# Kernel tuning notes

Hardware: AMD Instinct MI355X
Metric: run time of the kernel (lower is better)

Reference implementation:

```python
import jax, jax.numpy as jnp
import numpy as np

WSZ = 8          # window size (h == w)
DIM_HEAD = 32
EPS = 1e-5


def _rotate_half(t):
    t1, t2 = jnp.split(t, 2, axis=-1)
    return jnp.concatenate([-t2, t1], axis=-1)


def _window_rope(wsz_h, wsz_w, dim_head, base=10000.0):
    quarter = dim_head // 4
    freq = 1.0 / base ** (jnp.arange(quarter, dtype=jnp.float32) / quarter)
    th = jnp.arange(wsz_h, dtype=jnp.float32)[:, None] * freq[None, :]   # (wh, q)
    tw = jnp.arange(wsz_w, dtype=jnp.float32)[:, None] * freq[None, :]   # (ww, q)
    th = jnp.broadcast_to(th[:, None, :], (wsz_h, wsz_w, quarter)).reshape(wsz_h * wsz_w, quarter)
    tw = jnp.broadcast_to(tw[None, :, :], (wsz_h, wsz_w, quarter)).reshape(wsz_h * wsz_w, quarter)
    theta = jnp.concatenate([th, tw], axis=-1)                            # (L, d/2)
    cos = jnp.concatenate([jnp.cos(theta), jnp.cos(theta)], axis=-1)      # (L, d)
    sin = jnp.concatenate([jnp.sin(theta), jnp.sin(theta)], axis=-1)
    return cos, sin


def setup_inputs() -> dict:
    key = jax.random.key(0)
    k1, k2, k3 = jax.random.split(key, 3)
    B, D, H, W = 4, 512, 128, 128
    inner = 512  # heads * dim_head
    return {
        "x": jax.random.normal(k1, (B, D, H, W), dtype=jnp.float32),
        "ln_g": jnp.ones((D,), jnp.float32),
        "ln_b": jnp.zeros((D,), jnp.float32),
        "w_qkv": jax.random.normal(k2, (3 * inner, D), jnp.float32) * 0.02,
        "w_out": jax.random.normal(k3, (D, inner), jnp.float32) * 0.02,
        "b_out": jnp.zeros((D,), jnp.float32),
    }


def reference(x, ln_g, ln_b, w_qkv, w_out, b_out):
    B, D, H, W = x.shape
    wsz = WSZ
    dh = DIM_HEAD
    heads = D // dh
    nh, nw = H // wsz, W // wsz
    L = wsz * wsz
    shift = wsz // 2

    # channel LayerNorm (biased var over dim=1)
    mean = jnp.mean(x, axis=1, keepdims=True)
    var = jnp.var(x, axis=1, keepdims=True)
    xn = (x - mean) / jnp.sqrt(var + EPS) * ln_g[None, :, None, None] + ln_b[None, :, None, None]

    # shifted windows
    xs = jnp.roll(xn, shift=(-shift, -shift), axis=(-2, -1))
    # b d (h s1) (w s2) -> (b h w) d s1 s2
    xw = xs.reshape(B, D, nh, wsz, nw, wsz).transpose(0, 2, 4, 1, 3, 5)
    xw = xw.reshape(B * nh * nw, D, wsz, wsz)

    # 1x1 conv qkv (no bias)
    qkv = jnp.einsum('bdxy,ed->bexy', xw, w_qkv)           # (Bw, 3*inner, ws, ws)
    q, k, v = jnp.split(qkv, 3, axis=1)

    def to_heads(t):
        Bw = t.shape[0]
        return t.reshape(Bw, heads, dh, L).transpose(0, 1, 3, 2)  # (Bw, h, L, d)
    q, k, v = map(to_heads, (q, k, v))

    cos, sin = _window_rope(wsz, wsz, dh)
    cos = cos[None, None].astype(q.dtype)
    sin = sin[None, None].astype(q.dtype)
    q = q * cos + _rotate_half(q) * sin
    k = k * cos + _rotate_half(k) * sin

    scale = dh ** -0.5
    logits = jnp.einsum('bhid,bhjd->bhij', q, k) * scale
    attn = jax.nn.softmax(logits, axis=-1)
    out = jnp.einsum('bhij,bhjd->bhid', attn, v)            # (Bw, h, L, d)

    # b h (x y) d -> b (h d) x y
    out = out.transpose(0, 1, 3, 2).reshape(B * nh * nw, heads * dh, wsz, wsz)
    out = jnp.einsum('bdxy,ed->bexy', out, w_out) + b_out[None, :, None, None]

    # (b h w) d s1 s2 -> b d (h s1) (w s2)
    out = out.reshape(B, nh, nw, D, wsz, wsz).transpose(0, 3, 1, 4, 2, 5)
    out = out.reshape(B, D, H, W)
    out = jnp.roll(out, shift=(shift, shift), axis=(-2, -1))
    return out
```

## Files before the change

### kernel.cpp

```cpp
#include <hip/hip_runtime.h>
#include <hip/hip_bf16.h>

typedef unsigned short u16;
typedef __attribute__((ext_vector_type(8))) __bf16 bf16x8;
typedef __attribute__((ext_vector_type(4))) float f32x4;
typedef __attribute__((ext_vector_type(8))) unsigned short u16x8;

#define DEV __device__ __forceinline__

DEV float bf2f(u16 v){ union{unsigned u; float f;} c; c.u=((unsigned)v)<<16; return c.f; }
DEV u16 f2bf(float f){ union{float f; unsigned u;} c; c.f=f; unsigned r=c.u+0x7FFFu+((c.u>>16)&1u); return (u16)(r>>16); }
DEV f32x4 mfma16(bf16x8 a, bf16x8 b, f32x4 c){ return __builtin_amdgcn_mfma_f32_16x16x32_bf16(a,b,c,0,0,0); }


__global__ __launch_bounds__(256) void cvt_params_k(const float* __restrict__ wqkv, const float* __restrict__ wout,
                                                    const float* __restrict__ bout,
                                                    u16* __restrict__ wqkv_c, u16* __restrict__ wout_c,
                                                    u16* __restrict__ bout_c){
  int i = blockIdx.x*256 + threadIdx.x;
  if (i < 786432) wqkv_c[i] = f2bf(wqkv[i]);
  int j = i - 786432;
  if (j >= 0 && j < 262144) wout_c[j] = f2bf(wout[j]);
  int k = i - 1048576;
  if (k >= 0 && k < 512) bout_c[k] = f2bf(bout[k]);
}

__global__ __launch_bounds__(256) void ln_fused_k(const float* __restrict__ x, const float* __restrict__ g,
                                                  const float* __restrict__ bta, u16* __restrict__ A){
  __shared__ float sb[4][64], qb[4][64];
  const int blk = blockIdx.x;
  const int b = blk >> 8, rem = blk & 255;
  const int h_src = rem >> 1, w0 = (rem & 1) << 6;
  const int tid = threadIdx.x, dg = tid >> 6, lp = tid & 63;
  const float* xp = x + (((size_t)b*512)*128 + h_src)*128 + w0 + lp;
  const int dbase = dg*128;

  float s = 0.f, q = 0.f;
  #pragma unroll 8
  for (int d = 0; d < 128; ++d){
    float v = xp[(size_t)(dbase + d)*16384];
    s += v; q += v*v;
  }
  sb[dg][lp] = s; qb[dg][lp] = q;
  __syncthreads();
  float ts = sb[0][lp]+sb[1][lp]+sb[2][lp]+sb[3][lp];
  float tq = qb[0][lp]+qb[1][lp]+qb[2][lp]+qb[3][lp];
  float mean = ts*(1.f/512.f);
  float rstd = rsqrtf(tq*(1.f/512.f) - mean*mean + 1e-5f);

  const int w_src = w0 + lp;
  const int h_out = (h_src - 4) & 127, w_out = (w_src - 4) & 127;
  const int m = ((b*16 + (h_out>>3))*16 + (w_out>>3))*64 + (h_out&7)*8 + (w_out&7);
  u16* orow = A + (size_t)m*512 + dbase;

  for (int d0 = 0; d0 < 128; d0 += 8){
    u16x8 o;
    #pragma unroll
    for (int j = 0; j < 8; ++j){
      int d = dbase + d0 + j;
      float v = xp[(size_t)d*16384];
      o[j] = f2bf((v - mean)*rstd*g[d] + bta[d]);
    }
    *(u16x8*)(orow + d0) = o;
  }
}

template<bool BIAS>
__global__ __launch_bounds__(256) void gemm_nt_k(const u16* __restrict__ A, const u16* __restrict__ B,
                                                 const u16* __restrict__ bias, u16* __restrict__ C,
                                                 int M, int N, int K){
  __shared__ u16 As[128*32];
  __shared__ u16 Bs[128*32];
  const int tid = threadIdx.x, lane = tid & 63, wv = tid >> 6;
  const int q4 = lane >> 4, cc = lane & 15;
  const int m0 = blockIdx.y*128, n0 = blockIdx.x*128;
  const int wm = (wv >> 1)*64, wn = (wv & 1)*64;

  const int lrow = tid >> 2, lgrp = tid & 3;
  const u16* ag0 = A + (size_t)(m0 + lrow)*K + lgrp*8;
  const u16* ag1 = ag0 + (size_t)64*K;
  const u16* bg0 = B + (size_t)(n0 + lrow)*K + lgrp*8;
  const u16* bg1 = bg0 + (size_t)64*K;
  u16* as0 = As + tid*8;  u16* as1 = As + 2048 + tid*8;
  u16* bs0 = Bs + tid*8;  u16* bs1 = Bs + 2048 + tid*8;

  f32x4 acc[4][4] = {};
  for (int k0 = 0; k0 < K; k0 += 32){
    __builtin_amdgcn_global_load_lds(ag0 + k0, as0, 16, 0, 0);
    __builtin_amdgcn_global_load_lds(ag1 + k0, as1, 16, 0, 0);
    __builtin_amdgcn_global_load_lds(bg0 + k0, bs0, 16, 0, 0);
    __builtin_amdgcn_global_load_lds(bg1 + k0, bs1, 16, 0, 0);
    __syncthreads();
    bf16x8 af[4], bfr[4];
    #pragma unroll
    for (int t=0; t<4; ++t){
      u16x8 ta = *(const u16x8*)(As + (wm + t*16 + cc)*32 + q4*8);
      af[t]  = __builtin_bit_cast(bf16x8, ta);
      u16x8 tb = *(const u16x8*)(Bs + (wn + t*16 + cc)*32 + q4*8);
      bfr[t] = __builtin_bit_cast(bf16x8, tb);
    }
    #pragma unroll
    for (int i=0; i<4; ++i)
      #pragma unroll
      for (int j=0; j<4; ++j)
        acc[i][j] = mfma16(af[i], bfr[j], acc[i][j]);
    __syncthreads();
  }
  #pragma unroll
  for (int j=0; j<4; ++j){
    int col = n0 + wn + j*16 + cc;
    float bv = 0.f;
    if (BIAS) bv = bf2f(bias[col]);
    #pragma unroll
    for (int i=0; i<4; ++i){
      int rbase = m0 + wm + i*16 + q4*4;
      #pragma unroll
      for (int r=0; r<4; ++r)
        C[(size_t)(rbase + r)*N + col] = f2bf(acc[i][j][r] + bv);
    }
  }
}

__global__ __launch_bounds__(256) void attn_k(const u16* __restrict__ qkv, u16* __restrict__ O){
  __shared__ u16 Psh[4][64*72];
  const int tid = threadIdx.x, lane = tid & 63, wv = tid >> 6;
  const int q4 = lane >> 4, cc = lane & 15;
  const int w0 = blockIdx.x;
  const size_t base = (size_t)w0*64*1536;
  u16* Pw = Psh[wv];

  float freqj[8];
  #pragma unroll
  for (int j=0; j<8; ++j) freqj[j] = exp2f(-1.6609640474436811f * (float)j);
  const float sgn = (q4 < 2) ? -1.f : 1.f;
  const bool use_s2 = (q4 & 1) != 0;

  for (int hh=0; hh<4; ++hh){
    const int h = wv*4 + hh;
    bf16x8 qf[4], kf[4];
    #pragma unroll
    for (int t=0; t<4; ++t){
      const int l = t*16 + cc;
      const float sel = use_s2 ? (float)(l & 7) : (float)(l >> 3);
      u16x8 qr = *(const u16x8*)(qkv + base + (size_t)l*1536 + h*32 + q4*8);
      u16x8 kr = *(const u16x8*)(qkv + base + (size_t)l*1536 + 512 + h*32 + q4*8);
      u16x8 qo, ko;
      #pragma unroll
      for (int j=0; j<8; ++j){
        float qv = bf2f(qr[j]), kv = bf2f(kr[j]);
        float qp = __shfl_xor(qv, 32);
        float kp = __shfl_xor(kv, 32);
        float sn, cs; __sincosf(sel * freqj[j], &sn, &cs);
        qo[j] = f2bf(qv*cs + sgn*qp*sn);
        ko[j] = f2bf(kv*cs + sgn*kp*sn);
      }
      qf[t] = __builtin_bit_cast(bf16x8, qo);
      kf[t] = __builtin_bit_cast(bf16x8, ko);
    }
    f32x4 zero = {0.f, 0.f, 0.f, 0.f};
    f32x4 sacc[4][4];
    #pragma unroll
    for (int i=0; i<4; ++i)
      #pragma unroll
      for (int j=0; j<4; ++j)
        sacc[i][j] = mfma16(qf[i], kf[j], zero);
    const float scale = 0.17677669529663689f;
    #pragma unroll
    for (int i=0; i<4; ++i){
      #pragma unroll
      for (int r=0; r<4; ++r){
        float v0 = sacc[i][0][r]*scale, v1 = sacc[i][1][r]*scale;
        float v2 = sacc[i][2][r]*scale, v3 = sacc[i][3][r]*scale;
        float mx = fmaxf(fmaxf(v0,v1), fmaxf(v2,v3));
        #pragma unroll
        for (int msk=1; msk<16; msk<<=1) mx = fmaxf(mx, __shfl_xor(mx, msk));
        float e0 = __expf(v0-mx), e1 = __expf(v1-mx), e2 = __expf(v2-mx), e3 = __expf(v3-mx);
        float sm = e0+e1+e2+e3;
        #pragma unroll
        for (int msk=1; msk<16; msk<<=1) sm += __shfl_xor(sm, msk);
        float inv = 1.0f / sm;
        int row = i*16 + q4*4 + r;
        Pw[row*72 +      cc] = f2bf(e0*inv);
        Pw[row*72 + 16 + cc] = f2bf(e1*inv);
        Pw[row*72 + 32 + cc] = f2bf(e2*inv);
        Pw[row*72 + 48 + cc] = f2bf(e3*inv);
      }
    }
    __syncthreads();
    f32x4 oacc[4][2] = {};
    #pragma unroll
    for (int s=0; s<2; ++s){
      bf16x8 vf[2];
      #pragma unroll
      for (int tn=0; tn<2; ++tn){
        u16x8 vv;
        #pragma unroll
        for (int j=0; j<8; ++j){
          int jr = s*32 + q4*8 + j;
          vv[j] = qkv[base + (size_t)jr*1536 + 1024 + h*32 + tn*16 + cc];
        }
        vf[tn] = __builtin_bit_cast(bf16x8, vv);
      }
      #pragma unroll
      for (int i=0; i<4; ++i){
        u16x8 pp = *(const u16x8*)(Pw + (i*16 + cc)*72 + s*32 + q4*8);
        bf16x8 pf = __builtin_bit_cast(bf16x8, pp);
        oacc[i][0] = mfma16(pf, vf[0], oacc[i][0]);
        oacc[i][1] = mfma16(pf, vf[1], oacc[i][1]);
      }
    }
    #pragma unroll
    for (int i=0; i<4; ++i)
      #pragma unroll
      for (int tn=0; tn<2; ++tn)
        #pragma unroll
        for (int r=0; r<4; ++r)
          O[(size_t)(w0*64 + i*16 + q4*4 + r)*512 + h*32 + tn*16 + cc] = f2bf(oacc[i][tn][r]);
    __syncthreads();
  }
}

__global__ __launch_bounds__(256) void unpermute_k(const u16* __restrict__ Cm, float* __restrict__ out){
  __shared__ u16 T[64*130];
  const int tid = threadIdx.x;
  const int hb = blockIdx.x;
  const int b  = blockIdx.y;
  const int ih = hb >> 3, s1 = hb & 7;
  const int h_out = (hb + 4) & 127;
  const int rid = tid >> 1, half = tid & 1;
  const int iw = rid >> 3, s2 = rid & 7;
  const size_t m = ((size_t)((b*16 + ih)*16 + iw))*64 + s1*8 + s2;
  const u16* src = Cm + m*512 + half*32;
  const int dl = tid >> 2, wseg = tid & 3;

  for (int c0=0; c0<512; c0+=64){
    #pragma unroll
    for (int v=0; v<4; ++v){
      u16x8 r = *(const u16x8*)(src + c0 + v*8);
      #pragma unroll
      for (int j=0; j<8; ++j) T[(half*32 + v*8 + j)*130 + rid] = r[j];
    }
    __syncthreads();
    float* dst = out + (((size_t)(b*512 + c0 + dl))*128 + h_out)*128 + wseg*32;
    #pragma unroll
    for (int v=0; v<4; ++v){
      f32x4 o0, o1;
      #pragma unroll
      for (int j=0; j<4; ++j){
        int w = wseg*32 + v*8 + j;
        o0[j] = bf2f(T[dl*130 + ((w - 4) & 127)]);
      }
      #pragma unroll
      for (int j=0; j<4; ++j){
        int w = wseg*32 + v*8 + 4 + j;
        o1[j] = bf2f(T[dl*130 + ((w - 4) & 127)]);
      }
      *(f32x4*)(dst + v*8)     = o0;
      *(f32x4*)(dst + v*8 + 4) = o1;
    }
    __syncthreads();
  }
}

extern "C" void kernel_launch(void* const* d_in, const int* in_sizes, int n_in,
                              void* d_out, int out_size, void* d_ws, size_t ws_size,
                              hipStream_t stream){
  (void)in_sizes; (void)n_in; (void)out_size; (void)ws_size;
  const float* x     = (const float*)d_in[0];
  const float* ln_g  = (const float*)d_in[1];
  const float* ln_b  = (const float*)d_in[2];
  const float* w_qkv = (const float*)d_in[3];
  const float* w_out = (const float*)d_in[4];
  const float* b_out = (const float*)d_in[5];
  char* ws = (char*)d_ws;

  u16* A      = (u16*)ws;
  u16* QKVc   = (u16*)(ws + 67108864);
  u16* wqkv_c = (u16*)(ws + 2*67108864);
  u16* wout_c = (u16*)(ws + 2*67108864 + 1572864);
  u16* bout_c = (u16*)(ws + 2*67108864 + 1572864 + 524288);

  cvt_params_k<<<4099, 256, 0, stream>>>(w_qkv, w_out, b_out, wqkv_c, wout_c, bout_c);
  ln_fused_k  <<<1024, 256, 0, stream>>>(x, ln_g, ln_b, A);
  for (int c = 0; c < 4; ++c){
    u16* Ac = A + (size_t)c*16384*512;
    gemm_nt_k<false><<<dim3(12, 128), 256, 0, stream>>>(Ac, wqkv_c, (const u16*)nullptr, QKVc, 16384, 1536, 512);
    attn_k         <<<256, 256, 0, stream>>>(QKVc, Ac);
  }
  gemm_nt_k<true> <<<dim3(4, 512), 256, 0, stream>>>(A, wout_c, bout_c, QKVc, 65536, 512, 512);
  unpermute_k <<<dim3(128, 4), 256, 0, stream>>>(QKVc, (float*)d_out);
}
```

Measured before the change: 750.4 us.

## Vectorize LayerNorm loads and transpose through LDS for coalesced stores

The LayerNorm kernel now reads x with float4 loads across 16 channel rows per pass, reduces statistics through shared memory, and caches gamma/beta in LDS. Normalized values go into a padded shared tile, which is transposed so each thread writes 8 contiguous channels per output row. This targets the strided scalar loads and scattered 16-byte stores of the old kernel. In exchange it adds block barriers per 128-channel chunk and extra LDS traffic, and the padded 2-byte tile reads may cause bank conflicts.

```diff
diff --git a/kernel.cpp b/kernel.cpp
--- a/kernel.cpp
+++ b/kernel.cpp
@@ -27,41 +27,81 @@
 
 __global__ __launch_bounds__(256) void ln_fused_k(const float* __restrict__ x, const float* __restrict__ g,
                                                   const float* __restrict__ bta, u16* __restrict__ A){
-  __shared__ float sb[4][64], qb[4][64];
+  __shared__ float reds[16][64];
+  __shared__ float redq[16][64];
+  __shared__ float2 sstat[64];
+  __shared__ float sg[512], sb2[512];
+  __shared__ u16 tile[128*65];
+
   const int blk = blockIdx.x;
   const int b = blk >> 8, rem = blk & 255;
   const int h_src = rem >> 1, w0 = (rem & 1) << 6;
-  const int tid = threadIdx.x, dg = tid >> 6, lp = tid & 63;
-  const float* xp = x + (((size_t)b*512)*128 + h_src)*128 + w0 + lp;
-  const int dbase = dg*128;
-
-  float s = 0.f, q = 0.f;
+  const int tid = threadIdx.x;
+  const int wq = tid & 15, dr = tid >> 4;
+
+  sg[tid]        = g[tid];
+  sg[tid + 256]  = g[tid + 256];
+  sb2[tid]       = bta[tid];
+  sb2[tid + 256] = bta[tid + 256];
+
+  const float* xp = x + ((size_t)(b*512)*128 + h_src)*128 + w0 + wq*4;
+
+  float s0=0.f,s1=0.f,s2=0.f,s3=0.f, q0=0.f,q1=0.f,q2=0.f,q3=0.f;
   #pragma unroll 8
-  for (int d = 0; d < 128; ++d){
-    float v = xp[(size_t)(dbase + d)*16384];
-    s += v; q += v*v;
-  }
-  sb[dg][lp] = s; qb[dg][lp] = q;
+  for (int k = 0; k < 32; ++k){
+    float4 v = *(const float4*)(xp + (size_t)(k*16 + dr)*16384);
+    s0 += v.x; q0 += v.x*v.x;
+    s1 += v.y; q1 += v.y*v.y;
+    s2 += v.z; q2 += v.z*v.z;
+    s3 += v.w; q3 += v.w*v.w;
+  }
+  *(float4*)&reds[dr][wq*4] = make_float4(s0,s1,s2,s3);
+  *(float4*)&redq[dr][wq*4] = make_float4(q0,q1,q2,q3);
   __syncthreads();
-  float ts = sb[0][lp]+sb[1][lp]+sb[2][lp]+sb[3][lp];
-  float tq = qb[0][lp]+qb[1][lp]+qb[2][lp]+qb[3][lp];
-  float mean = ts*(1.f/512.f);
-  float rstd = rsqrtf(tq*(1.f/512.f) - mean*mean + 1e-5f);
-
-  const int w_src = w0 + lp;
-  const int h_out = (h_src - 4) & 127, w_out = (w_src - 4) & 127;
-  const int m = ((b*16 + (h_out>>3))*16 + (w_out>>3))*64 + (h_out&7)*8 + (w_out&7);
-  u16* orow = A + (size_t)m*512 + dbase;
-
-  for (int d0 = 0; d0 < 128; d0 += 8){
-    u16x8 o;
-    #pragma unroll
-    for (int j = 0; j < 8; ++j){
-      int d = dbase + d0 + j;
-      float v = xp[(size_t)d*16384];
-      o[j] = f2bf((v - mean)*rstd*g[d] + bta[d]);
-    }
-    *(u16x8*)(orow + d0) = o;
+
+  if (tid < 64){
+    float s = 0.f, q = 0.f;
+    #pragma unroll
+    for (int r = 0; r < 16; ++r){ s += reds[r][tid]; q += redq[r][tid]; }
+    float mean = s*(1.f/512.f);
+    float rstd = rsqrtf(q*(1.f/512.f) - mean*mean + 1e-5f);
+    sstat[tid] = make_float2(mean, rstd);
+  }
+  __syncthreads();
+
+  const float2 st0 = sstat[wq*4+0];
+  const float2 st1 = sstat[wq*4+1];
+  const float2 st2 = sstat[wq*4+2];
+  const float2 st3 = sstat[wq*4+3];
+
+  const int h_out = (h_src - 4) & 127;
+  const int mbase = ((b*16 + (h_out>>3))*16)*64 + (h_out&7)*8;
+  const int seg = tid & 15, i0 = tid >> 4;
+
+  for (int c = 0; c < 4; ++c){
+    #pragma unroll
+    for (int k = 0; k < 8; ++k){
+      const int d = c*128 + k*16 + dr;
+      float4 v = *(const float4*)(xp + (size_t)d*16384);
+      const float gg = sg[d], bb = sb2[d];
+      u16* tr = tile + (size_t)(k*16 + dr)*65 + wq*4;
+      tr[0] = f2bf((v.x - st0.x)*st0.y*gg + bb);
+      tr[1] = f2bf((v.y - st1.x)*st1.y*gg + bb);
+      tr[2] = f2bf((v.z - st2.x)*st2.y*gg + bb);
+      tr[3] = f2bf((v.w - st3.x)*st3.y*gg + bb);
+    }
+    __syncthreads();
+    #pragma unroll
+    for (int p = 0; p < 4; ++p){
+      const int i = p*16 + i0;
+      const int w_out = (w0 + i - 4) & 127;
+      const int m = mbase + (w_out>>3)*64 + (w_out&7);
+      u16x8 o;
+      #pragma unroll
+      for (int jj = 0; jj < 8; ++jj) o[jj] = tile[(size_t)(seg*8 + jj)*65 + i];
+      *(u16x8*)(A + (size_t)m*512 + c*128 + seg*8) = o;
+    }
+    __syncthreads();
   }
 }
 
```

Result: faster. 713.5 us (-4.9%).
